# Kernel optimization log

Measured on AMD Instinct MI355X. Metric: run time of the kernel, lower is better.

Reference implementation:

```python
import jax, jax.numpy as jnp
import numpy as np

N_NODES = 100000


def gcn_conv(x, src, dst, W, b, n_nodes):
    # PyG GCNConv: h = x @ W; add self-loops; symmetric norm; scatter-add; + bias
    h = x @ W  # [N, F_out]
    deg = jax.ops.segment_sum(jnp.ones_like(src, dtype=h.dtype), dst, num_segments=n_nodes)
    dinv = jnp.where(deg > 0, jax.lax.rsqrt(deg), 0.0)
    norm = dinv[src] * dinv[dst]  # [E+N]
    msgs = h[src] * norm[:, None]  # gather + scale
    out = jax.ops.segment_sum(msgs, dst, num_segments=n_nodes)  # scatter-add
    return out + b


def setup_inputs() -> dict:
    key = jax.random.key(0)
    ks = jax.random.split(key, 8)
    n, e, f_in, h = N_NODES, 1600000, 128, 64
    x = jax.random.normal(ks[0], (n, f_in), dtype=jnp.float32)
    edge_index = jax.random.randint(ks[1], (2, e), 0, n, dtype=jnp.int64)
    W1 = jax.random.normal(ks[2], (f_in, h), dtype=jnp.float32) / np.sqrt(f_in)
    b1 = jnp.zeros((h,), dtype=jnp.float32)
    W2 = jax.random.normal(ks[3], (h, h), dtype=jnp.float32) / np.sqrt(h)
    b2 = jnp.zeros((h,), dtype=jnp.float32)
    Wd = jax.random.normal(ks[4], (h, 1), dtype=jnp.float32) / np.sqrt(h)
    bd = jnp.zeros((1,), dtype=jnp.float32)
    return {"x": x, "edge_index": edge_index, "W1": W1, "b1": b1,
            "W2": W2, "b2": b2, "Wd": Wd, "bd": bd}


def reference(x, edge_index, W1, b1, W2, b2, Wd, bd):
    n = x.shape[0]
    loop = jnp.arange(n, dtype=edge_index.dtype)
    src = jnp.concatenate([edge_index[0], loop])  # add self-loops once
    dst = jnp.concatenate([edge_index[1], loop])
    h = jax.nn.relu(gcn_conv(x, src, dst, W1, b1, n))
    h = jax.nn.relu(gcn_conv(h, src, dst, W2, b2, n))
    return h @ Wd + bd
```

## Files before the change

### kernel.cpp

```cpp
#include <hip/hip_runtime.h>

#define NF 64
#define NBLK 256
#define SH 8
#define BMSK 255
#define MAXNB 2048

typedef unsigned short ushort_t;
typedef __attribute__((ext_vector_type(8))) short short8;
typedef __attribute__((ext_vector_type(4))) float f32x4;

__device__ inline ushort_t f2bf(float f) {
    unsigned u = __float_as_uint(f);
    return (ushort_t)((u + 0x7fffu + ((u >> 16) & 1u)) >> 16);
}
__device__ inline float bfhi(unsigned x) { return __uint_as_float(x & 0xffff0000u); }
__device__ inline float bflo(unsigned x) { return __uint_as_float(x << 16); }

#define PACK8(b, ua, ub) \
    b[0] = (short)f2bf(ua.x); b[1] = (short)f2bf(ua.y); \
    b[2] = (short)f2bf(ua.z); b[3] = (short)f2bf(ua.w); \
    b[4] = (short)f2bf(ub.x); b[5] = (short)f2bf(ub.y); \
    b[6] = (short)f2bf(ub.z); b[7] = (short)f2bf(ub.w);


__device__ inline int wave_incl_scan(int x, int lane) {
#pragma unroll
    for (int o = 1; o < 64; o <<= 1) { int y = __shfl_up(x, o, 64); if (lane >= o) x += y; }
    return x;
}

__global__ __launch_bounds__(256) void k_scan_a(const int* __restrict__ in, int* __restrict__ out,
                                                int* __restrict__ bsums, int n) {
    int t = threadIdx.x, lane = t & 63, wv = t >> 6;
    int base = blockIdx.x * 1024 + t * 4;
    int v[4]; int s = 0;
#pragma unroll
    for (int k = 0; k < 4; ++k) { int i = base + k; int x = (i < n) ? in[i] : 0; v[k] = s; s += x; }
    int incl = wave_incl_scan(s, lane);
    __shared__ int ws[4];
    if (lane == 63) ws[wv] = incl;
    __syncthreads();
    int wofs = 0;
#pragma unroll
    for (int w = 0; w < 4; ++w) if (w < wv) wofs += ws[w];
    int texcl = wofs + incl - s;
#pragma unroll
    for (int k = 0; k < 4; ++k) { int i = base + k; if (i < n) out[i] = texcl + v[k]; }
    if (t == 255) bsums[blockIdx.x] = wofs + incl;
}

__global__ __launch_bounds__(256) void k_scan_addb(int* __restrict__ data, const int* __restrict__ bsums,
                                                   int* __restrict__ bptr, int ntot, int E) {
    __shared__ int off_s;
    int t = threadIdx.x;
    int myChunk = (int)(blockIdx.x >> 2);
    if (t < 64) {
        int s = 0;
        for (int i = t; i < myChunk; i += 64) s += bsums[i];
#pragma unroll
        for (int o = 32; o > 0; o >>= 1) s += __shfl_xor(s, o, 64);
        if (t == 0) off_s = s;
    }
    __syncthreads();
    int off = off_s;
    int i = blockIdx.x * 256 + t;
    if (i < ntot) {
        int v = data[i] + off;
        data[i] = v;
        if ((i & (NBLK - 1)) == 0) bptr[i / NBLK] = v;
    }
    if (i == 0) bptr[ntot / NBLK] = E;
}


__global__ __launch_bounds__(256) void k_histA(const int* __restrict__ dst, int* __restrict__ hmat,
                                               int E, int NB, int chunk) {
    __shared__ int h[MAXNB];
    int blk = blockIdx.x;
    for (int i = threadIdx.x; i < NB; i += 256) h[i] = 0;
    __syncthreads();
    int beg = blk * chunk, end = beg + chunk; if (end > E) end = E;
    for (int e = beg + threadIdx.x; e < end; e += 256) atomicAdd(&h[dst[e] >> SH], 1);
    __syncthreads();
    for (int i = threadIdx.x; i < NB; i += 256) hmat[i * NBLK + blk] = h[i];
}

__global__ __launch_bounds__(256) void k_placeB(const int* __restrict__ src, const int* __restrict__ dst,
                                                const int* __restrict__ hmat, int* __restrict__ pairs,
                                                int E, int NB, int chunk) {
    __shared__ int cur[MAXNB];
    int blk = blockIdx.x;
    for (int i = threadIdx.x; i < NB; i += 256) cur[i] = hmat[i * NBLK + blk];
    __syncthreads();
    int beg = blk * chunk, end = beg + chunk; if (end > E) end = E;
    for (int e = beg + threadIdx.x; e < end; e += 256) {
        int s = src[e], d = dst[e];
        int off = atomicAdd(&cur[d >> SH], 1);
        pairs[off] = (s << SH) | (d & BMSK);
    }
}

__global__ __launch_bounds__(256) void k_csr(const int* __restrict__ bptr, const int* __restrict__ pairs,
                                             int* __restrict__ row_ptr, int* __restrict__ cnt,
                                             float* __restrict__ dinv, int* __restrict__ col, int n) {
    __shared__ int h[256];
    __shared__ int cur[256];
    __shared__ int ws[4];
    int b = blockIdx.x, t = threadIdx.x;
    h[t] = 0;
    __syncthreads();
    int beg = bptr[b], end = bptr[b + 1];
    for (int j = beg + t; j < end; j += 256) atomicAdd(&h[pairs[j] & BMSK], 1);
    __syncthreads();
    int c = h[t];
    int incl = wave_incl_scan(c, t & 63);
    if ((t & 63) == 63) ws[t >> 6] = incl;
    __syncthreads();
    int wofs = 0;
#pragma unroll
    for (int w = 0; w < 4; ++w) if (w < (t >> 6)) wofs += ws[w];
    int ex = wofs + incl - c;
    int node = (b << SH) + t;
    if (node < n) {
        row_ptr[node] = beg + ex;
        cnt[node] = c;
        dinv[node] = rsqrtf(1.0f + (float)c);
    }
    cur[t] = beg + ex;
    __syncthreads();
    for (int j = beg + t; j < end; j += 256) {
        int pk = pairs[j];
        int p = atomicAdd(&cur[pk & BMSK], 1);
        col[p] = pk >> SH;
    }
}

__global__ __launch_bounds__(256) void k_mm1(
    const float* __restrict__ X, const float* __restrict__ W,
    const float* __restrict__ dinv, ushort_t* __restrict__ out, int n)
{
    __shared__ ushort_t wf[16 * 512];
    int t = threadIdx.x;
    for (int idx = t; idx < 128 * 64; idx += 256) {
        int k = idx >> 6, c = idx & 63;
        int f = ((k >> 5) << 2) | (c >> 4);
        int ln = (c & 15) | (((k >> 3) & 3) << 4);
        wf[f * 512 + ln * 8 + (k & 7)] = f2bf(W[idx]);
    }
    __syncthreads();

    int lane = t & 63, wv = t >> 6;
    int r16 = lane & 15, kg = lane >> 4;
    int tile = blockIdx.x * 4 + wv;
    int row = tile * 16 + r16;
    int r = (row < n) ? row : (n - 1);
    const float* pX = X + (size_t)r * 128 + kg * 8;

    float4 u0a = *(const float4*)(pX + 0),   u0b = *(const float4*)(pX + 4);
    float4 u1a = *(const float4*)(pX + 32),  u1b = *(const float4*)(pX + 36);
    float4 u2a = *(const float4*)(pX + 64),  u2b = *(const float4*)(pX + 68);
    float4 u3a = *(const float4*)(pX + 96),  u3b = *(const float4*)(pX + 100);

    short8 b0, b1, b2, b3;
    PACK8(b0, u0a, u0b); PACK8(b1, u1a, u1b);
    PACK8(b2, u2a, u2b); PACK8(b3, u3a, u3b);

    short8 a0[4], a1[4], a2[4], a3[4];
#pragma unroll
    for (int f = 0; f < 4; ++f) {
        a0[f] = *(const short8*)(wf + (0 + f) * 512 + lane * 8);
        a1[f] = *(const short8*)(wf + (4 + f) * 512 + lane * 8);
        a2[f] = *(const short8*)(wf + (8 + f) * 512 + lane * 8);
        a3[f] = *(const short8*)(wf + (12 + f) * 512 + lane * 8);
    }

    f32x4 z = {0.f, 0.f, 0.f, 0.f};
    f32x4 acc[4];
#pragma unroll
    for (int f = 0; f < 4; ++f)
        acc[f] = __builtin_amdgcn_mfma_f32_16x16x32_bf16(a0[f], b0, z, 0, 0, 0);
#pragma unroll
    for (int f = 0; f < 4; ++f)
        acc[f] = __builtin_amdgcn_mfma_f32_16x16x32_bf16(a1[f], b1, acc[f], 0, 0, 0);
#pragma unroll
    for (int f = 0; f < 4; ++f)
        acc[f] = __builtin_amdgcn_mfma_f32_16x16x32_bf16(a2[f], b2, acc[f], 0, 0, 0);
#pragma unroll
    for (int f = 0; f < 4; ++f)
        acc[f] = __builtin_amdgcn_mfma_f32_16x16x32_bf16(a3[f], b3, acc[f], 0, 0, 0);

    if (row < n) {
        float di = dinv[row];
#pragma unroll
        for (int f = 0; f < 4; ++f) {
            ushort4 o;
            o.x = f2bf(acc[f][0] * di); o.y = f2bf(acc[f][1] * di);
            o.z = f2bf(acc[f][2] * di); o.w = f2bf(acc[f][3] * di);
            *(ushort4*)(out + (size_t)row * NF + f * 16 + kg * 4) = o;
        }
    }
}

__global__ __launch_bounds__(256) void k_mm2(
    const ushort_t* __restrict__ Xb, const float* __restrict__ W,
    const float* __restrict__ dinv, ushort_t* __restrict__ out, int n)
{
    __shared__ ushort_t wf[8 * 512];
    int t = threadIdx.x;
    for (int idx = t; idx < 64 * 64; idx += 256) {
        int k = idx >> 6, c = idx & 63;
        int f = ((k >> 5) << 2) | (c >> 4);
        int ln = (c & 15) | (((k >> 3) & 3) << 4);
        wf[f * 512 + ln * 8 + (k & 7)] = f2bf(W[idx]);
    }
    __syncthreads();

    int lane = t & 63, wv = t >> 6;
    short8 af[8];
#pragma unroll
    for (int f = 0; f < 8; ++f)
        af[f] = *(const short8*)(wf + f * 512 + lane * 8);

    int r16 = lane & 15, kg = lane >> 4;
    int tile0 = blockIdx.x * 8 + wv * 2;
    int rowA = tile0 * 16 + r16;
    int rowB = rowA + 16;
    int rA = (rowA < n) ? rowA : (n - 1);
    int rB = (rowB < n) ? rowB : (n - 1);

    const ushort_t* pA = Xb + (size_t)rA * NF + kg * 8;
    const ushort_t* pB = Xb + (size_t)rB * NF + kg * 8;
    short8 bA0 = *(const short8*)(pA);
    short8 bA1 = *(const short8*)(pA + 32);
    short8 bB0 = *(const short8*)(pB);
    short8 bB1 = *(const short8*)(pB + 32);

    f32x4 z = {0.f, 0.f, 0.f, 0.f};
    f32x4 accA[4], accB[4];
#pragma unroll
    for (int f = 0; f < 4; ++f) {
        accA[f] = __builtin_amdgcn_mfma_f32_16x16x32_bf16(af[f], bA0, z, 0, 0, 0);
        accA[f] = __builtin_amdgcn_mfma_f32_16x16x32_bf16(af[4 + f], bA1, accA[f], 0, 0, 0);
        accB[f] = __builtin_amdgcn_mfma_f32_16x16x32_bf16(af[f], bB0, z, 0, 0, 0);
        accB[f] = __builtin_amdgcn_mfma_f32_16x16x32_bf16(af[4 + f], bB1, accB[f], 0, 0, 0);
    }

    if (rowA < n) {
        float di = dinv[rowA];
#pragma unroll
        for (int f = 0; f < 4; ++f) {
            ushort4 o;
            o.x = f2bf(accA[f][0] * di); o.y = f2bf(accA[f][1] * di);
            o.z = f2bf(accA[f][2] * di); o.w = f2bf(accA[f][3] * di);
            *(ushort4*)(out + (size_t)rowA * NF + f * 16 + kg * 4) = o;
        }
    }
    if (rowB < n) {
        float di = dinv[rowB];
#pragma unroll
        for (int f = 0; f < 4; ++f) {
            ushort4 o;
            o.x = f2bf(accB[f][0] * di); o.y = f2bf(accB[f][1] * di);
            o.z = f2bf(accB[f][2] * di); o.w = f2bf(accB[f][3] * di);
            *(ushort4*)(out + (size_t)rowB * NF + f * 16 + kg * 4) = o;
        }
    }
}

template<bool DECODE>
__global__ __launch_bounds__(256) void k_pull(
    const ushort_t* __restrict__ hs, const float* __restrict__ dinv,
    const int* __restrict__ row_ptr, const int* __restrict__ cnt,
    const int* __restrict__ col, const float* __restrict__ bias,
    const float* __restrict__ Wd, const float* __restrict__ bd,
    void* __restrict__ outv, int n)
{
    int d = blockIdx.x * 16 + (threadIdx.x >> 4);
    if (d >= n) return;
    int lt = threadIdx.x & 15;
    int fo = lt << 2;
    int grpbase = threadIdx.x & 48;
    int beg = row_ptr[d], deg = cnt[d];

    uint2 sv = *((const uint2*)(hs + (size_t)d * NF) + lt);
    float4 acc = make_float4(bflo(sv.x), bfhi(sv.x), bflo(sv.y), bfhi(sv.y));

    for (int jb = 0; jb < deg; jb += 16) {
        int m = deg - jb; if (m > 16) m = 16;
        int idx = (lt < m) ? col[beg + jb + lt] : 0;
        uint2 v[16];
#pragma unroll
        for (int u = 0; u < 16; ++u) {
            int kk = (u < m) ? u : (m - 1);
            int s = __shfl(idx, grpbase + kk, 64);
            v[u] = *((const uint2*)(hs + (size_t)s * NF) + lt);
        }
#pragma unroll
        for (int u = 0; u < 16; ++u) {
            if (u < m) {
                acc.x += bflo(v[u].x); acc.y += bfhi(v[u].x);
                acc.z += bflo(v[u].y); acc.w += bfhi(v[u].y);
            }
        }
    }

    float di = dinv[d];
    float4 bv = *(const float4*)(bias + fo);
    float rx = fmaxf(fmaf(acc.x, di, bv.x), 0.0f);
    float ry = fmaxf(fmaf(acc.y, di, bv.y), 0.0f);
    float rz = fmaxf(fmaf(acc.z, di, bv.z), 0.0f);
    float rw = fmaxf(fmaf(acc.w, di, bv.w), 0.0f);

    if (DECODE) {
        float4 wv = *(const float4*)(Wd + fo);
        float vsum = rx * wv.x + ry * wv.y + rz * wv.z + rw * wv.w;
#pragma unroll
        for (int o = 1; o < 16; o <<= 1) vsum += __shfl_xor(vsum, o, 64);
        if (lt == 0) ((float*)outv)[d] = vsum + bd[0];
    } else {
        ushort4 o;
        o.x = f2bf(rx); o.y = f2bf(ry); o.z = f2bf(rz); o.w = f2bf(rw);
        *(ushort4*)((ushort_t*)outv + (size_t)d * NF + fo) = o;
    }
}

extern "C" void kernel_launch(void* const* d_in, const int* in_sizes, int n_in,
                              void* d_out, int out_size, void* d_ws, size_t ws_size,
                              hipStream_t stream) {
    const float* x  = (const float*)d_in[0];
    const int*   ei = (const int*)d_in[1];
    const float* W1 = (const float*)d_in[2];
    const float* b1 = (const float*)d_in[3];
    const float* W2 = (const float*)d_in[4];
    const float* b2 = (const float*)d_in[5];
    const float* Wd = (const float*)d_in[6];
    const float* bd = (const float*)d_in[7];
    float* out = (float*)d_out;

    int n = in_sizes[0] / 128;
    int E = in_sizes[1] / 2;
    const int* src = ei;
    const int* dst = ei + E;

    int NB = (n + (1 << SH) - 1) >> SH;
    int chunk = (E + NBLK - 1) / NBLK;
    int ntot = NB * NBLK;
    int nsb = (ntot + 1023) / 1024;
    int ntiles = (n + 15) / 16;

    float* dinv    = (float*)d_ws;
    float* bufH    = dinv + n;
    float* bufA    = bufH + (size_t)n * NF;
    int*   counts  = (int*)(bufA + (size_t)n * NF);
    int*   row_ptr = counts + n;
    int*   col     = row_ptr + n;
    int*   hmat    = col + E;
    int*   bptr    = hmat + ntot;
    int*   bsums   = bptr + NB + 1;
    int*   pairs   = (int*)bufH;
    ushort_t* hsb  = (ushort_t*)bufH;
    ushort_t* actb = (ushort_t*)bufA;

    k_histA<<<NBLK, 256, 0, stream>>>(dst, hmat, E, NB, chunk);
    k_scan_a<<<nsb, 256, 0, stream>>>(hmat, hmat, bsums, ntot);
    k_scan_addb<<<(ntot + 255) / 256, 256, 0, stream>>>(hmat, bsums, bptr, ntot, E);
    k_placeB<<<NBLK, 256, 0, stream>>>(src, dst, hmat, pairs, E, NB, chunk);

    k_csr<<<NB, 256, 0, stream>>>(bptr, pairs, row_ptr, counts, dinv, col, n);

    k_mm1<<<(ntiles + 3) / 4, 256, 0, stream>>>(x, W1, dinv, hsb, n);
    k_pull<false><<<(n + 15) / 16, 256, 0, stream>>>(hsb, dinv, row_ptr, counts, col, b1,
                                                     Wd, bd, actb, n);

    k_mm2<<<(ntiles + 7) / 8, 256, 0, stream>>>(actb, W2, dinv, hsb, n);
    k_pull<true><<<(n + 15) / 16, 256, 0, stream>>>(hsb, dinv, row_ptr, counts, col, b2,
                                                    Wd, bd, out, n);
}
```

Measured before the change: 141.7 us.

## Fuse layer-1 aggregation with layer-2 matmul into one kernel

Merges the first pull aggregation kernel and the second dense matmul into a single kernel. Each block gathers 16 destination rows, stages the ReLU activations in shared memory, and multiplies them by W2 with MFMA before writing the scaled hidden features. This removes one kernel launch and the global round trip of the intermediate activation buffer. In exchange, every block re-converts W2 into bf16 shared-memory layout, and each block does a small MFMA tile that may leave the matrix units underused.

```diff
diff --git a/kernel.cpp b/kernel.cpp
--- a/kernel.cpp
+++ b/kernel.cpp
@@ -202,11 +202,14 @@
     }
 }
 
-__global__ __launch_bounds__(256) void k_mm2(
-    const ushort_t* __restrict__ Xb, const float* __restrict__ W,
-    const float* __restrict__ dinv, ushort_t* __restrict__ out, int n)
+__global__ __launch_bounds__(256) void k_pullmm(
+    const ushort_t* __restrict__ hs, const float* __restrict__ dinv,
+    const int* __restrict__ row_ptr, const int* __restrict__ cnt,
+    const int* __restrict__ col, const float* __restrict__ bias,
+    const float* __restrict__ W, ushort_t* __restrict__ out, int n)
 {
     __shared__ ushort_t wf[8 * 512];
+    __shared__ ushort_t act[16][64];
     int t = threadIdx.x;
     for (int idx = t; idx < 64 * 64; idx += 256) {
         int k = idx >> 6, c = idx & 63;
@@ -214,67 +217,75 @@
         int ln = (c & 15) | (((k >> 3) & 3) << 4);
         wf[f * 512 + ln * 8 + (k & 7)] = f2bf(W[idx]);
     }
+
+    int d = blockIdx.x * 16 + (t >> 4);
+    int lt = t & 15;
+    int fo = lt << 2;
+    int grpbase = t & 48;
+    float rx = 0.f, ry = 0.f, rz = 0.f, rw = 0.f;
+    if (d < n) {
+        uint2 sv = *((const uint2*)(hs + (size_t)d * NF) + lt);
+        float4 acc = make_float4(bflo(sv.x), bfhi(sv.x), bflo(sv.y), bfhi(sv.y));
+        int beg = row_ptr[d], deg = cnt[d];
+        for (int jb = 0; jb < deg; jb += 16) {
+            int m = deg - jb; if (m > 16) m = 16;
+            int idx = (lt < m) ? col[beg + jb + lt] : 0;
+            uint2 v[16];
+#pragma unroll
+            for (int u = 0; u < 16; ++u) {
+                int kk = (u < m) ? u : (m - 1);
+                int s = __shfl(idx, grpbase + kk, 64);
+                v[u] = *((const uint2*)(hs + (size_t)s * NF) + lt);
+            }
+#pragma unroll
+            for (int u = 0; u < 16; ++u) {
+                if (u < m) {
+                    acc.x += bflo(v[u].x); acc.y += bfhi(v[u].x);
+                    acc.z += bflo(v[u].y); acc.w += bfhi(v[u].y);
+                }
+            }
+        }
+        float di = dinv[d];
+        float4 bv = *(const float4*)(bias + fo);
+        rx = fmaxf(fmaf(acc.x, di, bv.x), 0.0f);
+        ry = fmaxf(fmaf(acc.y, di, bv.y), 0.0f);
+        rz = fmaxf(fmaf(acc.z, di, bv.z), 0.0f);
+        rw = fmaxf(fmaf(acc.w, di, bv.w), 0.0f);
+    }
+    {
+        ushort4 o;
+        o.x = f2bf(rx); o.y = f2bf(ry); o.z = f2bf(rz); o.w = f2bf(rw);
+        *(ushort4*)(&act[t >> 4][fo]) = o;
+    }
     __syncthreads();
 
     int lane = t & 63, wv = t >> 6;
-    short8 af[8];
-#pragma unroll
-    for (int f = 0; f < 8; ++f)
-        af[f] = *(const short8*)(wf + f * 512 + lane * 8);
-
     int r16 = lane & 15, kg = lane >> 4;
-    int tile0 = blockIdx.x * 8 + wv * 2;
-    int rowA = tile0 * 16 + r16;
-    int rowB = rowA + 16;
-    int rA = (rowA < n) ? rowA : (n - 1);
-    int rB = (rowB < n) ? rowB : (n - 1);
-
-    const ushort_t* pA = Xb + (size_t)rA * NF + kg * 8;
-    const ushort_t* pB = Xb + (size_t)rB * NF + kg * 8;
-    short8 bA0 = *(const short8*)(pA);
-    short8 bA1 = *(const short8*)(pA + 32);
-    short8 bB0 = *(const short8*)(pB);
-    short8 bB1 = *(const short8*)(pB + 32);
+    short8 aflo = *(const short8*)(wf + wv * 512 + lane * 8);
+    short8 afhi = *(const short8*)(wf + (4 + wv) * 512 + lane * 8);
+    short8 bb0 = *(const short8*)(&act[r16][kg * 8]);
+    short8 bb1 = *(const short8*)(&act[r16][kg * 8 + 32]);
 
     f32x4 z = {0.f, 0.f, 0.f, 0.f};
-    f32x4 accA[4], accB[4];
-#pragma unroll
-    for (int f = 0; f < 4; ++f) {
-        accA[f] = __builtin_amdgcn_mfma_f32_16x16x32_bf16(af[f], bA0, z, 0, 0, 0);
-        accA[f] = __builtin_amdgcn_mfma_f32_16x16x32_bf16(af[4 + f], bA1, accA[f], 0, 0, 0);
-        accB[f] = __builtin_amdgcn_mfma_f32_16x16x32_bf16(af[f], bB0, z, 0, 0, 0);
-        accB[f] = __builtin_amdgcn_mfma_f32_16x16x32_bf16(af[4 + f], bB1, accB[f], 0, 0, 0);
-    }
-
-    if (rowA < n) {
-        float di = dinv[rowA];
-#pragma unroll
-        for (int f = 0; f < 4; ++f) {
-            ushort4 o;
-            o.x = f2bf(accA[f][0] * di); o.y = f2bf(accA[f][1] * di);
-            o.z = f2bf(accA[f][2] * di); o.w = f2bf(accA[f][3] * di);
-            *(ushort4*)(out + (size_t)rowA * NF + f * 16 + kg * 4) = o;
-        }
-    }
-    if (rowB < n) {
-        float di = dinv[rowB];
-#pragma unroll
-        for (int f = 0; f < 4; ++f) {
-            ushort4 o;
-            o.x = f2bf(accB[f][0] * di); o.y = f2bf(accB[f][1] * di);
-            o.z = f2bf(accB[f][2] * di); o.w = f2bf(accB[f][3] * di);
-            *(ushort4*)(out + (size_t)rowB * NF + f * 16 + kg * 4) = o;
-        }
-    }
-}
-
-template<bool DECODE>
-__global__ __launch_bounds__(256) void k_pull(
+    f32x4 acc2 = __builtin_amdgcn_mfma_f32_16x16x32_bf16(aflo, bb0, z, 0, 0, 0);
+    acc2 = __builtin_amdgcn_mfma_f32_16x16x32_bf16(afhi, bb1, acc2, 0, 0, 0);
+
+    int row = blockIdx.x * 16 + r16;
+    if (row < n) {
+        float di = dinv[row];
+        ushort4 o;
+        o.x = f2bf(acc2[0] * di); o.y = f2bf(acc2[1] * di);
+        o.z = f2bf(acc2[2] * di); o.w = f2bf(acc2[3] * di);
+        *(ushort4*)(out + (size_t)row * NF + wv * 16 + kg * 4) = o;
+    }
+}
+
+__global__ __launch_bounds__(256) void k_pull2(
     const ushort_t* __restrict__ hs, const float* __restrict__ dinv,
     const int* __restrict__ row_ptr, const int* __restrict__ cnt,
     const int* __restrict__ col, const float* __restrict__ bias,
     const float* __restrict__ Wd, const float* __restrict__ bd,
-    void* __restrict__ outv, int n)
+    float* __restrict__ outv, int n)
 {
     int d = blockIdx.x * 16 + (threadIdx.x >> 4);
     if (d >= n) return;
@@ -312,17 +323,11 @@
     float rz = fmaxf(fmaf(acc.z, di, bv.z), 0.0f);
     float rw = fmaxf(fmaf(acc.w, di, bv.w), 0.0f);
 
-    if (DECODE) {
-        float4 wv = *(const float4*)(Wd + fo);
-        float vsum = rx * wv.x + ry * wv.y + rz * wv.z + rw * wv.w;
-#pragma unroll
-        for (int o = 1; o < 16; o <<= 1) vsum += __shfl_xor(vsum, o, 64);
-        if (lt == 0) ((float*)outv)[d] = vsum + bd[0];
-    } else {
-        ushort4 o;
-        o.x = f2bf(rx); o.y = f2bf(ry); o.z = f2bf(rz); o.w = f2bf(rw);
-        *(ushort4*)((ushort_t*)outv + (size_t)d * NF + fo) = o;
-    }
+    float4 wv = *(const float4*)(Wd + fo);
+    float vsum = rx * wv.x + ry * wv.y + rz * wv.z + rw * wv.w;
+#pragma unroll
+    for (int o = 1; o < 16; o <<= 1) vsum += __shfl_xor(vsum, o, 64);
+    if (lt == 0) outv[d] = vsum + bd[0];
 }
 
 extern "C" void kernel_launch(void* const* d_in, const int* in_sizes, int n_in,
@@ -360,7 +365,7 @@
     int*   bsums   = bptr + NB + 1;
     int*   pairs   = (int*)bufH;
     ushort_t* hsb  = (ushort_t*)bufH;
-    ushort_t* actb = (ushort_t*)bufA;
+    ushort_t* hs2b = (ushort_t*)bufA;
 
     k_histA<<<NBLK, 256, 0, stream>>>(dst, hmat, E, NB, chunk);
     k_scan_a<<<nsb, 256, 0, stream>>>(hmat, hmat, bsums, ntot);
@@ -370,10 +375,10 @@
     k_csr<<<NB, 256, 0, stream>>>(bptr, pairs, row_ptr, counts, dinv, col, n);
 
     k_mm1<<<(ntiles + 3) / 4, 256, 0, stream>>>(x, W1, dinv, hsb, n);
-    k_pull<false><<<(n + 15) / 16, 256, 0, stream>>>(hsb, dinv, row_ptr, counts, col, b1,
-                                                     Wd, bd, actb, n);
-
-    k_mm2<<<(ntiles + 7) / 8, 256, 0, stream>>>(actb, W2, dinv, hsb, n);
-    k_pull<true><<<(n + 15) / 16, 256, 0, stream>>>(hsb, dinv, row_ptr, counts, col, b2,
-                                                    Wd, bd, out, n);
-}
+
+    k_pullmm<<<(n + 15) / 16, 256, 0, stream>>>(hsb, dinv, row_ptr, counts, col, b1,
+                                                W2, hs2b, n);
+
+    k_pull2<<<(n + 15) / 16, 256, 0, stream>>>(hs2b, dinv, row_ptr, counts, col, b2,
+                                               Wd, bd, out, n);
+}
```

Result: faster. 134.0 us (-5.5%).
